# Kernel optimization log

Hardware: AMD Instinct MI355X
Metric: run time of the kernel (lower is better)

The kernel has to match this reference:

```python
import jax, jax.numpy as jnp
import numpy as np

# Dims: batch=64, n_cols=512, n_e=80, n_i=20, embed=512
DT_OVER_TAU = 0.1  # leaky rate-neuron integration constant (dt/tau)

B, C, NE, NI, E = 64, 512, 80, 20, 512


def setup_inputs() -> dict:
    key = jax.random.key(0)
    ks = jax.random.split(key, 12)
    return {
        "thal": jax.random.normal(ks[0], (B, E), jnp.float32),
        "thal_increments": jax.random.normal(ks[1], (B, C, E), jnp.float32),
        "l23_fb": jax.random.normal(ks[2], (B, C, NE), jnp.float32),
        # state (rates nonnegative, membrane potentials gaussian)
        "r_e": jax.random.uniform(ks[3], (B, C, NE), jnp.float32),
        "r_i": jax.random.uniform(ks[4], (B, C, NI), jnp.float32),
        "e_v": jax.random.normal(ks[5], (B, C, NE), jnp.float32),
        "i_v": jax.random.normal(ks[6], (B, C, NI), jnp.float32),
        # learned params (per-column weight stacks)
        "input_proj": jax.random.normal(ks[7], (C, NE, E), jnp.float32) * (1.0 / np.sqrt(E).astype(np.float32)),
        "feedback_proj": jax.random.normal(ks[8], (C, NE, NE), jnp.float32) * (1.0 / np.sqrt(NE).astype(np.float32)),
        # static synapses: nonnegative weights, sign handled by E/I convention
        "W_ee": jax.random.uniform(ks[9], (C, NE, NE), jnp.float32) * (1.0 / np.sqrt(NE).astype(np.float32)),
        "W_ei": jax.random.uniform(ks[10], (C, NI, NE), jnp.float32) * (1.0 / np.sqrt(NE).astype(np.float32)),
        "W_ie": jax.random.uniform(ks[11], (C, NE, NI), jnp.float32) * (1.0 / np.sqrt(NI).astype(np.float32)),
    }


def reference(thal, thal_increments, l23_fb, r_e, r_i, e_v, i_v,
              input_proj, feedback_proj, W_ee, W_ei, W_ie):
    # thal [B,E] broadcast over columns + per-column increments -> [B,C,E]
    thal_full = thal[:, None, :] + thal_increments
    # external + feedback drive onto excitatory pop: [B,C,NE]
    I_ext = jnp.einsum('bce,coe->bco', thal_full, input_proj)
    I_fb = jnp.einsum('bce,coe->bco', l23_fb, feedback_proj)
    # synapse currents (static weights; E->E, E->I excitatory, I->E inhibitory)
    I_ee = jnp.einsum('bcp,cop->bco', r_e, W_ee)   # [B,C,NE]
    I_ei = jnp.einsum('bcp,cop->bco', r_e, W_ei)   # [B,C,NI]
    I_ie = -jnp.einsum('bcp,cop->bco', r_i, W_ie)  # [B,C,NE], inhibitory
    I_e_total = I_ext + I_fb + I_ee + I_ie
    I_i_total = I_ei
    # leaky rate-neuron state update: v <- v + dt/tau * (-v + I); r = relu(v)
    v_e_new = e_v + DT_OVER_TAU * (I_e_total - e_v)
    v_i_new = i_v + DT_OVER_TAU * (I_i_total - i_v)
    r_e_new = jax.nn.relu(v_e_new)
    r_i_new = jax.nn.relu(v_i_new)
    # (layer_outputs e_out/l23_out/l5_out all alias r_e_new; return new state too)
    return r_e_new, r_i_new, v_e_new, v_i_new
```

## Files before the change

kernel.cpp:

```cpp
#include <hip/hip_runtime.h>
#include <hip/hip_bf16.h>

typedef __attribute__((ext_vector_type(8))) short bf16x8;
typedef __attribute__((ext_vector_type(4))) float f32x4;
typedef unsigned short u16;

__device__ __forceinline__ u16 f2bf(float f) {
  __hip_bfloat16 h = __float2bfloat16(f);
  u16 u;
  __builtin_memcpy(&u, &h, 2);
  return u;
}
__device__ __forceinline__ void cvt4_store(u16* dst, float4 v) {
  u16 rr[4] = {f2bf(v.x), f2bf(v.y), f2bf(v.z), f2bf(v.w)};
  uint2 p;
  __builtin_memcpy(&p, rr, 8);
  *(uint2*)dst = p;
}


__global__ __launch_bounds__(256, 4) void ei_cols_mfma(
    const float* __restrict__ thal,
    const float* __restrict__ inc,
    const float* __restrict__ l23,
    const float* __restrict__ re_in,
    const float* __restrict__ ri_in,
    const float* __restrict__ ev_in,
    const float* __restrict__ iv_in,
    const float* __restrict__ in_proj,
    const float* __restrict__ fb_proj,
    const float* __restrict__ w_ee,
    const float* __restrict__ w_ei,
    const float* __restrict__ w_ie,
    float* __restrict__ out)
{
  __shared__ __align__(16) unsigned char smem[32256];
  const int c = blockIdx.x;
  const int bh32 = blockIdx.y * 32;
  const int tid = threadIdx.x;
  const int lane = tid & 63;
  const int wave = tid >> 6;
  const int nidx = lane & 15;
  const int quad = lane >> 4;
  const int mw = wave & 1;
  const int jh = wave >> 1;
  const int m0 = mw * 16;

  f32x4 acc_e[3], acc_i[2];
#pragma unroll
  for (int j = 0; j < 3; ++j) acc_e[j] = (f32x4){0.f, 0.f, 0.f, 0.f};
#pragma unroll
  for (int j = 0; j < 2; ++j) acc_i[j] = (f32x4){0.f, 0.f, 0.f, 0.f};

  {
    float4 tv[2], gv[2], wv[5];

    auto load_regs = [&](int k0) {
#pragma unroll
      for (int j = 0; j < 2; ++j) {
        int l = tid + j * 256;
        int b = l >> 4, kk = (l & 15) << 2;
        tv[j] = *(const float4*)(thal + (bh32 + b) * 512 + k0 + kk);
        gv[j] = *(const float4*)(inc + (size_t)(bh32 + b) * 262144 +
                                 (size_t)c * 512 + k0 + kk);
      }
#pragma unroll
      for (int j = 0; j < 5; ++j) {
        int l = tid + j * 256;
        int o = l >> 4, kk = (l & 15) << 2;
        wv[j] = *(const float4*)(in_proj + (size_t)c * 40960 + o * 512 + k0 + kk);
      }
    };
    auto store_buf = [&](int p) {
      u16* A = (u16*)(smem + p * 16128);
      u16* W = (u16*)(smem + 4608 + p * 16128);
#pragma unroll
      for (int j = 0; j < 2; ++j) {
        int l = tid + j * 256;
        int b = l >> 4, kk = (l & 15) << 2;
        float4 s;
        s.x = tv[j].x + gv[j].x; s.y = tv[j].y + gv[j].y;
        s.z = tv[j].z + gv[j].z; s.w = tv[j].w + gv[j].w;
        cvt4_store(A + b * 72 + kk, s);
      }
#pragma unroll
      for (int j = 0; j < 5; ++j) {
        int l = tid + j * 256;
        int o = l >> 4, kk = (l & 15) << 2;
        cvt4_store(W + o * 72 + kk, wv[j]);
      }
    };

    load_regs(0);
    store_buf(0);
    for (int i = 0; i < 8; ++i) {
      __syncthreads();
      if (i < 7) load_regs((i + 1) * 64);
      const int p = i & 1;
      const u16* A = (const u16*)(smem + p * 16128);
      const u16* W = (const u16*)(smem + 4608 + p * 16128);
#pragma unroll
      for (int kk0 = 0; kk0 < 64; kk0 += 32) {
        bf16x8 a = *(const bf16x8*)(A + (m0 + nidx) * 72 + kk0 + quad * 8);
        if (jh == 0) {
#pragma unroll
          for (int j = 0; j < 3; ++j) {
            bf16x8 b = *(const bf16x8*)(W + (j * 16 + nidx) * 72 + kk0 + quad * 8);
            acc_e[j] = __builtin_amdgcn_mfma_f32_16x16x32_bf16(a, b, acc_e[j], 0, 0, 0);
          }
        } else {
#pragma unroll
          for (int j = 0; j < 2; ++j) {
            bf16x8 b = *(const bf16x8*)(W + ((j + 3) * 16 + nidx) * 72 + kk0 + quad * 8);
            acc_e[j] = __builtin_amdgcn_mfma_f32_16x16x32_bf16(a, b, acc_e[j], 0, 0, 0);
          }
        }
      }
      if (i < 7) store_buf((i + 1) & 1);
    }
  }

  {
    __syncthreads();
    u16* As = (u16*)smem;
    u16* Bs = (u16*)(smem + 6656);
    for (int l = tid; l < 640; l += 256) {
      int b = l / 20, kk = (l % 20) << 2;
      cvt4_store(As + b * 104 + kk,
                 *(const float4*)(l23 + ((size_t)(bh32 + b) * 512 + c) * 80 + kk));
    }
    for (int l = tid; l < 64; l += 256) {
      int b = l >> 1, off = 80 + (l & 1) * 8;
      *(uint4*)(As + b * 104 + off) = (uint4){0u, 0u, 0u, 0u};
    }
    for (int l = tid; l < 1600; l += 256) {
      int o = l / 20, kk = (l % 20) << 2;
      cvt4_store(Bs + o * 104 + kk,
                 *(const float4*)(fb_proj + ((size_t)c * 80 + o) * 80 + kk));
    }
    for (int l = tid; l < 160; l += 256) {
      int o = l >> 1, off = 80 + (l & 1) * 8;
      *(uint4*)(Bs + o * 104 + off) = (uint4){0u, 0u, 0u, 0u};
    }
    __syncthreads();
#pragma unroll
    for (int kk0 = 0; kk0 < 96; kk0 += 32) {
      bf16x8 a = *(const bf16x8*)(As + (m0 + nidx) * 104 + kk0 + quad * 8);
      if (jh == 0) {
#pragma unroll
        for (int j = 0; j < 3; ++j) {
          bf16x8 b = *(const bf16x8*)(Bs + (j * 16 + nidx) * 104 + kk0 + quad * 8);
          acc_e[j] = __builtin_amdgcn_mfma_f32_16x16x32_bf16(a, b, acc_e[j], 0, 0, 0);
        }
      } else {
#pragma unroll
        for (int j = 0; j < 2; ++j) {
          bf16x8 b = *(const bf16x8*)(Bs + ((j + 3) * 16 + nidx) * 104 + kk0 + quad * 8);
          acc_e[j] = __builtin_amdgcn_mfma_f32_16x16x32_bf16(a, b, acc_e[j], 0, 0, 0);
        }
      }
    }
  }

  {
    __syncthreads();
    u16* As = (u16*)smem;
    u16* W1 = (u16*)(smem + 6656);
    u16* W2 = (u16*)(smem + 23296);
    for (int l = tid; l < 640; l += 256) {
      int b = l / 20, kk = (l % 20) << 2;
      cvt4_store(As + b * 104 + kk,
                 *(const float4*)(re_in + ((size_t)(bh32 + b) * 512 + c) * 80 + kk));
    }
    for (int l = tid; l < 64; l += 256) {
      int b = l >> 1, off = 80 + (l & 1) * 8;
      *(uint4*)(As + b * 104 + off) = (uint4){0u, 0u, 0u, 0u};
    }
    for (int l = tid; l < 1600; l += 256) {
      int o = l / 20, kk = (l % 20) << 2;
      cvt4_store(W1 + o * 104 + kk,
                 *(const float4*)(w_ee + ((size_t)c * 80 + o) * 80 + kk));
    }
    for (int l = tid; l < 160; l += 256) {
      int o = l >> 1, off = 80 + (l & 1) * 8;
      *(uint4*)(W1 + o * 104 + off) = (uint4){0u, 0u, 0u, 0u};
    }
    for (int l = tid; l < 400; l += 256) {
      int o = l / 20, kk = (l % 20) << 2;
      cvt4_store(W2 + o * 104 + kk,
                 *(const float4*)(w_ei + ((size_t)c * 20 + o) * 80 + kk));
    }
    for (int l = tid; l < 40; l += 256) {
      int o = l >> 1, off = 80 + (l & 1) * 8;
      *(uint4*)(W2 + o * 104 + off) = (uint4){0u, 0u, 0u, 0u};
    }
    for (int l = tid; l < 144; l += 256) {
      int o = 20 + l / 12, off = (l % 12) * 8;
      *(uint4*)(W2 + o * 104 + off) = (uint4){0u, 0u, 0u, 0u};
    }
    __syncthreads();
#pragma unroll
    for (int kk0 = 0; kk0 < 96; kk0 += 32) {
      bf16x8 a = *(const bf16x8*)(As + (m0 + nidx) * 104 + kk0 + quad * 8);
      if (jh == 0) {
#pragma unroll
        for (int j = 0; j < 3; ++j) {
          bf16x8 b = *(const bf16x8*)(W1 + (j * 16 + nidx) * 104 + kk0 + quad * 8);
          acc_e[j] = __builtin_amdgcn_mfma_f32_16x16x32_bf16(a, b, acc_e[j], 0, 0, 0);
        }
      } else {
#pragma unroll
        for (int j = 0; j < 2; ++j) {
          bf16x8 b = *(const bf16x8*)(W1 + ((j + 3) * 16 + nidx) * 104 + kk0 + quad * 8);
          acc_e[j] = __builtin_amdgcn_mfma_f32_16x16x32_bf16(a, b, acc_e[j], 0, 0, 0);
        }
#pragma unroll
        for (int j = 0; j < 2; ++j) {
          bf16x8 b = *(const bf16x8*)(W2 + (j * 16 + nidx) * 104 + kk0 + quad * 8);
          acc_i[j] = __builtin_amdgcn_mfma_f32_16x16x32_bf16(a, b, acc_i[j], 0, 0, 0);
        }
      }
    }
  }

  float evr[3][4], ivr[2][4];
  {
    __syncthreads();
    u16* Ri = (u16*)smem;
    u16* Wn = (u16*)(smem + 2560);
    for (int l = tid; l < 160; l += 256) {
      int b = l / 5, kk = (l % 5) << 2;
      cvt4_store(Ri + b * 40 + kk,
                 *(const float4*)(ri_in + ((size_t)(bh32 + b) * 512 + c) * 20 + kk));
    }
    for (int l = tid; l < 96; l += 256) {
      int b = l / 3, kk = 20 + (l % 3) * 4;
      *(uint2*)(Ri + b * 40 + kk) = (uint2){0u, 0u};
    }
    for (int l = tid; l < 400; l += 256) {
      int o = l / 5, kk = (l % 5) << 2;
      float4 v = *(const float4*)(w_ie + ((size_t)c * 80 + o) * 20 + kk);
      v.x = -v.x; v.y = -v.y; v.z = -v.z; v.w = -v.w;
      cvt4_store(Wn + o * 40 + kk, v);
    }
    for (int l = tid; l < 240; l += 256) {
      int o = l / 3, kk = 20 + (l % 3) * 4;
      *(uint2*)(Wn + o * 40 + kk) = (uint2){0u, 0u};
    }

    {
      const int row0 = bh32 + m0 + quad * 4;
      if (jh == 0) {
#pragma unroll
        for (int j = 0; j < 3; ++j) {
          int col = j * 16 + nidx;
#pragma unroll
          for (int r = 0; r < 4; ++r)
            evr[j][r] = ev_in[((size_t)(row0 + r) * 512 + c) * 80 + col];
        }
      } else {
#pragma unroll
        for (int j = 0; j < 2; ++j) {
          int col = (j + 3) * 16 + nidx;
#pragma unroll
          for (int r = 0; r < 4; ++r)
            evr[j][r] = ev_in[((size_t)(row0 + r) * 512 + c) * 80 + col];
        }
#pragma unroll
        for (int j = 0; j < 2; ++j) {
          int col = j * 16 + nidx;
#pragma unroll
          for (int r = 0; r < 4; ++r)
            ivr[j][r] = (col < 20)
                ? iv_in[((size_t)(row0 + r) * 512 + c) * 20 + col] : 0.f;
        }
      }
    }

    __syncthreads();
    {
      bf16x8 a = *(const bf16x8*)(Ri + (m0 + nidx) * 40 + quad * 8);
      if (jh == 0) {
#pragma unroll
        for (int j = 0; j < 3; ++j) {
          bf16x8 b = *(const bf16x8*)(Wn + (j * 16 + nidx) * 40 + quad * 8);
          acc_e[j] = __builtin_amdgcn_mfma_f32_16x16x32_bf16(a, b, acc_e[j], 0, 0, 0);
        }
      } else {
#pragma unroll
        for (int j = 0; j < 2; ++j) {
          bf16x8 b = *(const bf16x8*)(Wn + ((j + 3) * 16 + nidx) * 40 + quad * 8);
          acc_e[j] = __builtin_amdgcn_mfma_f32_16x16x32_bf16(a, b, acc_e[j], 0, 0, 0);
        }
      }
    }
  }

  {
    const size_t R_ri = 2621440u;
    const size_t R_ve = 3276800u;
    const size_t R_vi = 5898240u;
    const int row0 = bh32 + m0 + quad * 4;
    if (jh == 0) {
#pragma unroll
      for (int j = 0; j < 3; ++j) {
        int col = j * 16 + nidx;
#pragma unroll
        for (int r = 0; r < 4; ++r) {
          size_t g = ((size_t)(row0 + r) * 512 + c) * 80 + col;
          float e0 = evr[j][r];
          float v = e0 + 0.1f * (acc_e[j][r] - e0);
          out[g] = fmaxf(v, 0.f);
          out[R_ve + g] = v;
        }
      }
    } else {
#pragma unroll
      for (int j = 0; j < 2; ++j) {
        int col = (j + 3) * 16 + nidx;
#pragma unroll
        for (int r = 0; r < 4; ++r) {
          size_t g = ((size_t)(row0 + r) * 512 + c) * 80 + col;
          float e0 = evr[j][r];
          float v = e0 + 0.1f * (acc_e[j][r] - e0);
          out[g] = fmaxf(v, 0.f);
          out[R_ve + g] = v;
        }
      }
#pragma unroll
      for (int j = 0; j < 2; ++j) {
        int col = j * 16 + nidx;
        if (col < 20) {
#pragma unroll
          for (int r = 0; r < 4; ++r) {
            size_t g = ((size_t)(row0 + r) * 512 + c) * 20 + col;
            float i0 = ivr[j][r];
            float v = i0 + 0.1f * (acc_i[j][r] - i0);
            out[R_ri + g] = fmaxf(v, 0.f);
            out[R_vi + g] = v;
          }
        }
      }
    }
  }
}

extern "C" void kernel_launch(void* const* d_in, const int* in_sizes, int n_in,
                              void* d_out, int out_size, void* d_ws, size_t ws_size,
                              hipStream_t stream) {
  const float* thal = (const float*)d_in[0];
  const float* inc = (const float*)d_in[1];
  const float* l23 = (const float*)d_in[2];
  const float* re = (const float*)d_in[3];
  const float* ri = (const float*)d_in[4];
  const float* ev = (const float*)d_in[5];
  const float* iv = (const float*)d_in[6];
  const float* in_proj = (const float*)d_in[7];
  const float* fb_proj = (const float*)d_in[8];
  const float* w_ee = (const float*)d_in[9];
  const float* w_ei = (const float*)d_in[10];
  const float* w_ie = (const float*)d_in[11];
  float* out = (float*)d_out;
  ei_cols_mfma<<<dim3(512, 2), dim3(256), 0, stream>>>(
      thal, inc, l23, re, ri, ev, iv, in_proj, fb_proj, w_ee, w_ei, w_ie, out);
}
```

Measured before the change: 258.2 us.

## Merge batch halves into one block and load weights directly into MFMA registers

Each block now covers all 64 batch rows of a column with 512 threads, replacing the two 32-row blocks per column. Each column's weights are therefore fetched once rather than twice. The weight operands for all four matmuls are read from global memory straight into MFMA B-fragments and converted to bf16 in registers, so the shared-memory staging of weights and its extra syncs go away. Activation tiles get a deeper register prefetch, and the l23/re/ri loads are overlapped with earlier compute. The cost is uncoalesced per-lane weight loads, fewer blocks (512), and 512-thread launch bounds that may raise register pressure.

```diff
diff --git a/kernel.cpp b/kernel.cpp
--- a/kernel.cpp
+++ b/kernel.cpp
@@ -17,9 +17,16 @@
   __builtin_memcpy(&p, rr, 8);
   *(uint2*)dst = p;
 }
-
-
-__global__ __launch_bounds__(256, 4) void ei_cols_mfma(
+__device__ __forceinline__ bf16x8 pack8(float4 a, float4 b) {
+  u16 h[8] = {f2bf(a.x), f2bf(a.y), f2bf(a.z), f2bf(a.w),
+              f2bf(b.x), f2bf(b.y), f2bf(b.z), f2bf(b.w)};
+  bf16x8 r;
+  __builtin_memcpy(&r, h, 16);
+  return r;
+}
+
+
+__global__ __launch_bounds__(512, 4) void ei_cols_mfma(
     const float* __restrict__ thal,
     const float* __restrict__ inc,
     const float* __restrict__ l23,
@@ -34,16 +41,15 @@
     const float* __restrict__ w_ie,
     float* __restrict__ out)
 {
-  __shared__ __align__(16) unsigned char smem[32256];
+  __shared__ __align__(16) unsigned char smem[31744];
   const int c = blockIdx.x;
-  const int bh32 = blockIdx.y * 32;
   const int tid = threadIdx.x;
   const int lane = tid & 63;
   const int wave = tid >> 6;
   const int nidx = lane & 15;
   const int quad = lane >> 4;
-  const int mw = wave & 1;
-  const int jh = wave >> 1;
+  const int mw = wave & 3;
+  const int jh = wave >> 2;
   const int m0 = mw * 16;
 
   f32x4 acc_e[3], acc_i[2];
@@ -52,246 +58,260 @@
 #pragma unroll
   for (int j = 0; j < 2; ++j) acc_i[j] = (f32x4){0.f, 0.f, 0.f, 0.f};
 
-  {
-    float4 tv[2], gv[2], wv[5];
-
-    auto load_regs = [&](int k0) {
-#pragma unroll
-      for (int j = 0; j < 2; ++j) {
-        int l = tid + j * 256;
-        int b = l >> 4, kk = (l & 15) << 2;
-        tv[j] = *(const float4*)(thal + (bh32 + b) * 512 + k0 + kk);
-        gv[j] = *(const float4*)(inc + (size_t)(bh32 + b) * 262144 +
-                                 (size_t)c * 512 + k0 + kk);
-      }
-#pragma unroll
-      for (int j = 0; j < 5; ++j) {
-        int l = tid + j * 256;
-        int o = l >> 4, kk = (l & 15) << 2;
-        wv[j] = *(const float4*)(in_proj + (size_t)c * 40960 + o * 512 + k0 + kk);
-      }
-    };
-    auto store_buf = [&](int p) {
-      u16* A = (u16*)(smem + p * 16128);
-      u16* W = (u16*)(smem + 4608 + p * 16128);
-#pragma unroll
-      for (int j = 0; j < 2; ++j) {
-        int l = tid + j * 256;
-        int b = l >> 4, kk = (l & 15) << 2;
-        float4 s;
-        s.x = tv[j].x + gv[j].x; s.y = tv[j].y + gv[j].y;
-        s.z = tv[j].z + gv[j].z; s.w = tv[j].w + gv[j].w;
-        cvt4_store(A + b * 72 + kk, s);
-      }
-#pragma unroll
-      for (int j = 0; j < 5; ++j) {
-        int l = tid + j * 256;
-        int o = l >> 4, kk = (l & 15) << 2;
-        cvt4_store(W + o * 72 + kk, wv[j]);
-      }
-    };
-
-    load_regs(0);
-    store_buf(0);
-    for (int i = 0; i < 8; ++i) {
-      __syncthreads();
-      if (i < 7) load_regs((i + 1) * 64);
-      const int p = i & 1;
-      const u16* A = (const u16*)(smem + p * 16128);
-      const u16* W = (const u16*)(smem + 4608 + p * 16128);
-#pragma unroll
-      for (int kk0 = 0; kk0 < 64; kk0 += 32) {
-        bf16x8 a = *(const bf16x8*)(A + (m0 + nidx) * 72 + kk0 + quad * 8);
-        if (jh == 0) {
-#pragma unroll
-          for (int j = 0; j < 3; ++j) {
-            bf16x8 b = *(const bf16x8*)(W + (j * 16 + nidx) * 72 + kk0 + quad * 8);
-            acc_e[j] = __builtin_amdgcn_mfma_f32_16x16x32_bf16(a, b, acc_e[j], 0, 0, 0);
-          }
-        } else {
-#pragma unroll
-          for (int j = 0; j < 2; ++j) {
-            bf16x8 b = *(const bf16x8*)(W + ((j + 3) * 16 + nidx) * 72 + kk0 + quad * 8);
-            acc_e[j] = __builtin_amdgcn_mfma_f32_16x16x32_bf16(a, b, acc_e[j], 0, 0, 0);
-          }
-        }
-      }
-      if (i < 7) store_buf((i + 1) & 1);
-    }
-  }
-
-  {
+  const float* wA = in_proj + (size_t)c * 40960;
+
+  float4 tv0[2], gv0[2], tv1[2], gv1[2];
+  float4 fbv[3];
+
+  auto loadA = [&](float4* tv, float4* gv, int k0) {
+#pragma unroll
+    for (int j = 0; j < 2; ++j) {
+      int l = tid + j * 512;
+      int b = l >> 4, kk = (l & 15) << 2;
+      tv[j] = *(const float4*)(thal + b * 512 + k0 + kk);
+      gv[j] = *(const float4*)(inc + (size_t)b * 262144 + (size_t)c * 512 + k0 + kk);
+    }
+  };
+  auto storeA = [&](int p, float4* tv, float4* gv) {
+    u16* A = (u16*)(smem + p * 9216);
+#pragma unroll
+    for (int j = 0; j < 2; ++j) {
+      int l = tid + j * 512;
+      int b = l >> 4, kk = (l & 15) << 2;
+      float4 s;
+      s.x = tv[j].x + gv[j].x; s.y = tv[j].y + gv[j].y;
+      s.z = tv[j].z + gv[j].z; s.w = tv[j].w + gv[j].w;
+      cvt4_store(A + b * 72 + kk, s);
+    }
+  };
+
+  loadA(tv0, gv0, 0);
+  storeA(0, tv0, gv0);
+  loadA(tv1, gv1, 64);
+  loadA(tv0, gv0, 128);
+
+  for (int i = 0; i < 8; ++i) {
     __syncthreads();
-    u16* As = (u16*)smem;
-    u16* Bs = (u16*)(smem + 6656);
-    for (int l = tid; l < 640; l += 256) {
+    const int p1 = (i + 1) & 1;
+    if (i < 7) {
+      if (p1) storeA(1, tv1, gv1); else storeA(0, tv0, gv0);
+    }
+    if (i < 5) {
+      if (p1) loadA(tv1, gv1, (i + 3) * 64); else loadA(tv0, gv0, (i + 3) * 64);
+    }
+    if (i == 5) {
+#pragma unroll
+      for (int j = 0; j < 3; ++j) {
+        int l = tid + j * 512;
+        if (l < 1280) {
+          int b = l / 20, kk = (l % 20) << 2;
+          fbv[j] = *(const float4*)(l23 + ((size_t)b * 512 + c) * 80 + kk);
+        }
+      }
+    }
+    if (i == 7) {
+      u16* As = (u16*)(smem + 18432);
+#pragma unroll
+      for (int j = 0; j < 3; ++j) {
+        int l = tid + j * 512;
+        if (l < 1280) {
+          int b = l / 20, kk = (l % 20) << 2;
+          cvt4_store(As + b * 104 + kk, fbv[j]);
+        }
+      }
+      if (tid < 128) {
+        int b = tid >> 1, off = 80 + (tid & 1) * 8;
+        *(uint4*)(As + b * 104 + off) = (uint4){0u, 0u, 0u, 0u};
+      }
+    }
+    const u16* A = (const u16*)(smem + (i & 1) * 9216);
+    const float* wb = wA + i * 64;
+#pragma unroll
+    for (int kk0 = 0; kk0 < 64; kk0 += 32) {
+      bf16x8 a = *(const bf16x8*)(A + (m0 + nidx) * 72 + kk0 + quad * 8);
+      if (jh == 0) {
+#pragma unroll
+        for (int j = 0; j < 3; ++j) {
+          const float* p = wb + (size_t)(j * 16 + nidx) * 512 + kk0 + quad * 8;
+          bf16x8 b = pack8(*(const float4*)p, *(const float4*)(p + 4));
+          acc_e[j] = __builtin_amdgcn_mfma_f32_16x16x32_bf16(a, b, acc_e[j], 0, 0, 0);
+        }
+      } else {
+#pragma unroll
+        for (int j = 0; j < 2; ++j) {
+          const float* p = wb + (size_t)((3 + j) * 16 + nidx) * 512 + kk0 + quad * 8;
+          bf16x8 b = pack8(*(const float4*)p, *(const float4*)(p + 4));
+          acc_e[j] = __builtin_amdgcn_mfma_f32_16x16x32_bf16(a, b, acc_e[j], 0, 0, 0);
+        }
+      }
+    }
+  }
+
+  float4 rev[3];
+#pragma unroll
+  for (int j = 0; j < 3; ++j) {
+    int l = tid + j * 512;
+    if (l < 1280) {
       int b = l / 20, kk = (l % 20) << 2;
-      cvt4_store(As + b * 104 + kk,
-                 *(const float4*)(l23 + ((size_t)(bh32 + b) * 512 + c) * 80 + kk));
-    }
-    for (int l = tid; l < 64; l += 256) {
-      int b = l >> 1, off = 80 + (l & 1) * 8;
-      *(uint4*)(As + b * 104 + off) = (uint4){0u, 0u, 0u, 0u};
-    }
-    for (int l = tid; l < 1600; l += 256) {
-      int o = l / 20, kk = (l % 20) << 2;
-      cvt4_store(Bs + o * 104 + kk,
-                 *(const float4*)(fb_proj + ((size_t)c * 80 + o) * 80 + kk));
-    }
-    for (int l = tid; l < 160; l += 256) {
-      int o = l >> 1, off = 80 + (l & 1) * 8;
-      *(uint4*)(Bs + o * 104 + off) = (uint4){0u, 0u, 0u, 0u};
-    }
-    __syncthreads();
+      rev[j] = *(const float4*)(re_in + ((size_t)b * 512 + c) * 80 + kk);
+    }
+  }
+  __syncthreads();
+  {
+    const u16* As = (const u16*)(smem + 18432);
+    const float* fb = fb_proj + (size_t)c * 6400;
 #pragma unroll
     for (int kk0 = 0; kk0 < 96; kk0 += 32) {
       bf16x8 a = *(const bf16x8*)(As + (m0 + nidx) * 104 + kk0 + quad * 8);
+      const bool full = (kk0 < 64) || (quad < 2);
       if (jh == 0) {
 #pragma unroll
         for (int j = 0; j < 3; ++j) {
-          bf16x8 b = *(const bf16x8*)(Bs + (j * 16 + nidx) * 104 + kk0 + quad * 8);
+          const float* p = fb + (size_t)(j * 16 + nidx) * 80 + kk0 + quad * 8;
+          float4 w0 = {0.f, 0.f, 0.f, 0.f}, w1 = {0.f, 0.f, 0.f, 0.f};
+          if (full) { w0 = *(const float4*)p; w1 = *(const float4*)(p + 4); }
+          bf16x8 b = pack8(w0, w1);
           acc_e[j] = __builtin_amdgcn_mfma_f32_16x16x32_bf16(a, b, acc_e[j], 0, 0, 0);
         }
       } else {
 #pragma unroll
         for (int j = 0; j < 2; ++j) {
-          bf16x8 b = *(const bf16x8*)(Bs + ((j + 3) * 16 + nidx) * 104 + kk0 + quad * 8);
-          acc_e[j] = __builtin_amdgcn_mfma_f32_16x16x32_bf16(a, b, acc_e[j], 0, 0, 0);
-        }
-      }
-    }
-  }
-
-  {
-    __syncthreads();
-    u16* As = (u16*)smem;
-    u16* W1 = (u16*)(smem + 6656);
-    u16* W2 = (u16*)(smem + 23296);
-    for (int l = tid; l < 640; l += 256) {
-      int b = l / 20, kk = (l % 20) << 2;
-      cvt4_store(As + b * 104 + kk,
-                 *(const float4*)(re_in + ((size_t)(bh32 + b) * 512 + c) * 80 + kk));
-    }
-    for (int l = tid; l < 64; l += 256) {
-      int b = l >> 1, off = 80 + (l & 1) * 8;
-      *(uint4*)(As + b * 104 + off) = (uint4){0u, 0u, 0u, 0u};
-    }
-    for (int l = tid; l < 1600; l += 256) {
-      int o = l / 20, kk = (l % 20) << 2;
-      cvt4_store(W1 + o * 104 + kk,
-                 *(const float4*)(w_ee + ((size_t)c * 80 + o) * 80 + kk));
-    }
-    for (int l = tid; l < 160; l += 256) {
-      int o = l >> 1, off = 80 + (l & 1) * 8;
-      *(uint4*)(W1 + o * 104 + off) = (uint4){0u, 0u, 0u, 0u};
-    }
-    for (int l = tid; l < 400; l += 256) {
-      int o = l / 20, kk = (l % 20) << 2;
-      cvt4_store(W2 + o * 104 + kk,
-                 *(const float4*)(w_ei + ((size_t)c * 20 + o) * 80 + kk));
-    }
-    for (int l = tid; l < 40; l += 256) {
-      int o = l >> 1, off = 80 + (l & 1) * 8;
-      *(uint4*)(W2 + o * 104 + off) = (uint4){0u, 0u, 0u, 0u};
-    }
-    for (int l = tid; l < 144; l += 256) {
-      int o = 20 + l / 12, off = (l % 12) * 8;
-      *(uint4*)(W2 + o * 104 + off) = (uint4){0u, 0u, 0u, 0u};
-    }
-    __syncthreads();
+          const float* p = fb + (size_t)((3 + j) * 16 + nidx) * 80 + kk0 + quad * 8;
+          float4 w0 = {0.f, 0.f, 0.f, 0.f}, w1 = {0.f, 0.f, 0.f, 0.f};
+          if (full) { w0 = *(const float4*)p; w1 = *(const float4*)(p + 4); }
+          bf16x8 b = pack8(w0, w1);
+          acc_e[j] = __builtin_amdgcn_mfma_f32_16x16x32_bf16(a, b, acc_e[j], 0, 0, 0);
+        }
+      }
+    }
+  }
+
+  __syncthreads();
+  {
+    u16* Asw = (u16*)(smem + 18432);
+#pragma unroll
+    for (int j = 0; j < 3; ++j) {
+      int l = tid + j * 512;
+      if (l < 1280) {
+        int b = l / 20, kk = (l % 20) << 2;
+        cvt4_store(Asw + b * 104 + kk, rev[j]);
+      }
+    }
+    if (tid < 128) {
+      int b = tid >> 1, off = 80 + (tid & 1) * 8;
+      *(uint4*)(Asw + b * 104 + off) = (uint4){0u, 0u, 0u, 0u};
+    }
+  }
+  float4 riv;
+  if (tid < 320) {
+    int b = tid / 5, kk = (tid % 5) << 2;
+    riv = *(const float4*)(ri_in + ((size_t)b * 512 + c) * 20 + kk);
+  }
+  __syncthreads();
+  {
+    const u16* As = (const u16*)(smem + 18432);
+    const float* wee = w_ee + (size_t)c * 6400;
+    const float* wei = w_ei + (size_t)c * 1600;
 #pragma unroll
     for (int kk0 = 0; kk0 < 96; kk0 += 32) {
       bf16x8 a = *(const bf16x8*)(As + (m0 + nidx) * 104 + kk0 + quad * 8);
+      const bool full = (kk0 < 64) || (quad < 2);
       if (jh == 0) {
 #pragma unroll
         for (int j = 0; j < 3; ++j) {
-          bf16x8 b = *(const bf16x8*)(W1 + (j * 16 + nidx) * 104 + kk0 + quad * 8);
+          const float* p = wee + (size_t)(j * 16 + nidx) * 80 + kk0 + quad * 8;
+          float4 w0 = {0.f, 0.f, 0.f, 0.f}, w1 = {0.f, 0.f, 0.f, 0.f};
+          if (full) { w0 = *(const float4*)p; w1 = *(const float4*)(p + 4); }
+          bf16x8 b = pack8(w0, w1);
           acc_e[j] = __builtin_amdgcn_mfma_f32_16x16x32_bf16(a, b, acc_e[j], 0, 0, 0);
         }
       } else {
 #pragma unroll
         for (int j = 0; j < 2; ++j) {
-          bf16x8 b = *(const bf16x8*)(W1 + ((j + 3) * 16 + nidx) * 104 + kk0 + quad * 8);
+          const float* p = wee + (size_t)((3 + j) * 16 + nidx) * 80 + kk0 + quad * 8;
+          float4 w0 = {0.f, 0.f, 0.f, 0.f}, w1 = {0.f, 0.f, 0.f, 0.f};
+          if (full) { w0 = *(const float4*)p; w1 = *(const float4*)(p + 4); }
+          bf16x8 b = pack8(w0, w1);
           acc_e[j] = __builtin_amdgcn_mfma_f32_16x16x32_bf16(a, b, acc_e[j], 0, 0, 0);
         }
 #pragma unroll
         for (int j = 0; j < 2; ++j) {
-          bf16x8 b = *(const bf16x8*)(W2 + (j * 16 + nidx) * 104 + kk0 + quad * 8);
+          int row = j * 16 + nidx;
+          float4 w0 = {0.f, 0.f, 0.f, 0.f}, w1 = {0.f, 0.f, 0.f, 0.f};
+          if (row < 20 && full) {
+            const float* p = wei + (size_t)row * 80 + kk0 + quad * 8;
+            w0 = *(const float4*)p; w1 = *(const float4*)(p + 4);
+          }
+          bf16x8 b = pack8(w0, w1);
           acc_i[j] = __builtin_amdgcn_mfma_f32_16x16x32_bf16(a, b, acc_i[j], 0, 0, 0);
         }
       }
     }
   }
 
+  __syncthreads();
+  {
+    u16* Ri = (u16*)(smem + 18432);
+    if (tid < 320) {
+      int b = tid / 5, kk = (tid % 5) << 2;
+      cvt4_store(Ri + b * 40 + kk, riv);
+    }
+    if (tid < 192) {
+      int b = tid / 3, kk = 20 + (tid % 3) * 4;
+      *(uint2*)(Ri + b * 40 + kk) = (uint2){0u, 0u};
+    }
+  }
   float evr[3][4], ivr[2][4];
-  {
-    __syncthreads();
-    u16* Ri = (u16*)smem;
-    u16* Wn = (u16*)(smem + 2560);
-    for (int l = tid; l < 160; l += 256) {
-      int b = l / 5, kk = (l % 5) << 2;
-      cvt4_store(Ri + b * 40 + kk,
-                 *(const float4*)(ri_in + ((size_t)(bh32 + b) * 512 + c) * 20 + kk));
-    }
-    for (int l = tid; l < 96; l += 256) {
-      int b = l / 3, kk = 20 + (l % 3) * 4;
-      *(uint2*)(Ri + b * 40 + kk) = (uint2){0u, 0u};
-    }
-    for (int l = tid; l < 400; l += 256) {
-      int o = l / 5, kk = (l % 5) << 2;
-      float4 v = *(const float4*)(w_ie + ((size_t)c * 80 + o) * 20 + kk);
-      v.x = -v.x; v.y = -v.y; v.z = -v.z; v.w = -v.w;
-      cvt4_store(Wn + o * 40 + kk, v);
-    }
-    for (int l = tid; l < 240; l += 256) {
-      int o = l / 3, kk = 20 + (l % 3) * 4;
-      *(uint2*)(Wn + o * 40 + kk) = (uint2){0u, 0u};
-    }
-
-    {
-      const int row0 = bh32 + m0 + quad * 4;
-      if (jh == 0) {
-#pragma unroll
-        for (int j = 0; j < 3; ++j) {
-          int col = j * 16 + nidx;
-#pragma unroll
-          for (int r = 0; r < 4; ++r)
-            evr[j][r] = ev_in[((size_t)(row0 + r) * 512 + c) * 80 + col];
-        }
-      } else {
-#pragma unroll
-        for (int j = 0; j < 2; ++j) {
-          int col = (j + 3) * 16 + nidx;
-#pragma unroll
-          for (int r = 0; r < 4; ++r)
-            evr[j][r] = ev_in[((size_t)(row0 + r) * 512 + c) * 80 + col];
-        }
-#pragma unroll
-        for (int j = 0; j < 2; ++j) {
-          int col = j * 16 + nidx;
-#pragma unroll
-          for (int r = 0; r < 4; ++r)
-            ivr[j][r] = (col < 20)
-                ? iv_in[((size_t)(row0 + r) * 512 + c) * 20 + col] : 0.f;
-        }
-      }
-    }
-
-    __syncthreads();
-    {
-      bf16x8 a = *(const bf16x8*)(Ri + (m0 + nidx) * 40 + quad * 8);
-      if (jh == 0) {
-#pragma unroll
-        for (int j = 0; j < 3; ++j) {
-          bf16x8 b = *(const bf16x8*)(Wn + (j * 16 + nidx) * 40 + quad * 8);
-          acc_e[j] = __builtin_amdgcn_mfma_f32_16x16x32_bf16(a, b, acc_e[j], 0, 0, 0);
-        }
-      } else {
-#pragma unroll
-        for (int j = 0; j < 2; ++j) {
-          bf16x8 b = *(const bf16x8*)(Wn + ((j + 3) * 16 + nidx) * 40 + quad * 8);
-          acc_e[j] = __builtin_amdgcn_mfma_f32_16x16x32_bf16(a, b, acc_e[j], 0, 0, 0);
-        }
+  const int row0 = m0 + quad * 4;
+  if (jh == 0) {
+#pragma unroll
+    for (int j = 0; j < 3; ++j) {
+      int col = j * 16 + nidx;
+#pragma unroll
+      for (int r = 0; r < 4; ++r)
+        evr[j][r] = ev_in[((size_t)(row0 + r) * 512 + c) * 80 + col];
+    }
+  } else {
+#pragma unroll
+    for (int j = 0; j < 2; ++j) {
+      int col = 48 + j * 16 + nidx;
+#pragma unroll
+      for (int r = 0; r < 4; ++r)
+        evr[j][r] = ev_in[((size_t)(row0 + r) * 512 + c) * 80 + col];
+    }
+#pragma unroll
+    for (int j = 0; j < 2; ++j) {
+      int col = j * 16 + nidx;
+#pragma unroll
+      for (int r = 0; r < 4; ++r)
+        ivr[j][r] = (col < 20)
+            ? iv_in[((size_t)(row0 + r) * 512 + c) * 20 + col] : 0.f;
+    }
+  }
+  __syncthreads();
+  {
+    const u16* Ri = (const u16*)(smem + 18432);
+    bf16x8 a = *(const bf16x8*)(Ri + (m0 + nidx) * 40 + quad * 8);
+    auto wieF = [&](int row) -> bf16x8 {
+      const float* p = w_ie + (size_t)c * 1600 + row * 20 + quad * 8;
+      float4 w0 = {0.f, 0.f, 0.f, 0.f}, w1 = {0.f, 0.f, 0.f, 0.f};
+      if (quad < 2) { w0 = *(const float4*)p; w1 = *(const float4*)(p + 4); }
+      else if (quad == 2) { w0 = *(const float4*)p; }
+      w0.x = -w0.x; w0.y = -w0.y; w0.z = -w0.z; w0.w = -w0.w;
+      w1.x = -w1.x; w1.y = -w1.y; w1.z = -w1.z; w1.w = -w1.w;
+      return pack8(w0, w1);
+    };
+    if (jh == 0) {
+#pragma unroll
+      for (int j = 0; j < 3; ++j) {
+        bf16x8 b = wieF(j * 16 + nidx);
+        acc_e[j] = __builtin_amdgcn_mfma_f32_16x16x32_bf16(a, b, acc_e[j], 0, 0, 0);
+      }
+    } else {
+#pragma unroll
+      for (int j = 0; j < 2; ++j) {
+        bf16x8 b = wieF((3 + j) * 16 + nidx);
+        acc_e[j] = __builtin_amdgcn_mfma_f32_16x16x32_bf16(a, b, acc_e[j], 0, 0, 0);
       }
     }
   }
@@ -300,7 +320,6 @@
     const size_t R_ri = 2621440u;
     const size_t R_ve = 3276800u;
     const size_t R_vi = 5898240u;
-    const int row0 = bh32 + m0 + quad * 4;
     if (jh == 0) {
 #pragma unroll
       for (int j = 0; j < 3; ++j) {
@@ -317,7 +336,7 @@
     } else {
 #pragma unroll
       for (int j = 0; j < 2; ++j) {
-        int col = (j + 3) * 16 + nidx;
+        int col = 48 + j * 16 + nidx;
 #pragma unroll
         for (int r = 0; r < 4; ++r) {
           size_t g = ((size_t)(row0 + r) * 512 + c) * 80 + col;
@@ -361,6 +380,6 @@
   const float* w_ei = (const float*)d_in[10];
   const float* w_ie = (const float*)d_in[11];
   float* out = (float*)d_out;
-  ei_cols_mfma<<<dim3(512, 2), dim3(256), 0, stream>>>(
+  ei_cols_mfma<<<dim3(512), dim3(512), 0, stream>>>(
       thal, inc, l23, re, ri, ev, iv, in_proj, fb_proj, w_ee, w_ei, w_ie, out);
 }
```

Measured after the change: 259.2 us. About the same (+0.4%).
